# Performance work log

Measured on AMD Instinct MI355X. Metric: run time of the kernel, lower is better.

Reference implementation:

```python
import jax, jax.numpy as jnp
import numpy as np

GROUP_SIZES = np.array([64, 48, 56, 40, 32, 24, 16, 8])
N_GROUPS = 8
MAX_GS = 64
D_MODEL = 2048
BATCH = 8192


def setup_inputs() -> dict:
    key = jax.random.key(0)
    k1, k2, k3, k4 = jax.random.split(key, 4)
    hidden = jax.random.normal(k1, (BATCH, N_GROUPS, D_MODEL), dtype=jnp.float32)
    chosen = jax.random.randint(k2, (BATCH,), 0, N_GROUPS)
    scale = 1.0 / np.sqrt(D_MODEL)  # nn.Linear default init range
    W = jax.random.uniform(k3, (N_GROUPS, MAX_GS, D_MODEL), minval=-scale, maxval=scale, dtype=jnp.float32)
    b = jax.random.uniform(k4, (N_GROUPS, MAX_GS), minval=-scale, maxval=scale, dtype=jnp.float32)
    gs = jnp.asarray(GROUP_SIZES, dtype=jnp.int32)
    # zero-pad decoder rows beyond each group's true output size
    row_mask = jnp.arange(MAX_GS)[None, :] < gs[:, None]  # [G, MAX_GS]
    W = W * row_mask[:, :, None]
    b = b * row_mask
    return {"hidden": hidden, "chosen_group_idx": chosen, "W": W, "b": b, "group_sizes": gs}


def reference(hidden, chosen_group_idx, W, b, group_sizes):
    # hidden: [B, G, D]; chosen_group_idx: [B]; W: [G, MAX_GS, D] (zero-padded); b: [G, MAX_GS]
    # Gather each sample's chosen group slice: [B, D]
    h = jnp.take_along_axis(hidden, chosen_group_idx[:, None, None], axis=1)[:, 0, :]
    Wg = W[chosen_group_idx]  # [B, MAX_GS, D]
    bg = b[chosen_group_idx]  # [B, MAX_GS]
    preds = jnp.einsum('bd,bgd->bg', h, Wg) + bg  # [B, MAX_GS]
    valid = jnp.arange(W.shape[1])[None, :] < group_sizes[chosen_group_idx][:, None]
    preds = jnp.where(valid, preds, 0.0)  # padded slots are zero, as in the torch module
    return preds, valid
```

## Files before the change

kernel.cpp:

```cpp
#include <hip/hip_runtime.h>
#include <hip/hip_bf16.h>

#define BATCH   8192
#define NGRP    8
#define MAXGS   64
#define DMODEL  2048
#define TM      16
#define TILES   (BATCH / TM)
#define NBLK    32
#define NKK     (DMODEL / 32)

typedef __attribute__((ext_vector_type(8))) short  short8;
typedef __attribute__((ext_vector_type(4))) float  f32x4;
typedef __attribute__((ext_vector_type(4))) short  short4v;

#define CNT_OFF   0
#define HIST_OFF  512
#define BASES_OFF 1536
#define LISTS_OFF 4096
#define W_OFF     (LISTS_OFF + NGRP * BATCH * 4)
#define CNT_STRIDE 16

static __device__ __forceinline__ short bf(float f) {
    __hip_bfloat16 h = __float2bfloat16(f);
    return (short)__bfloat16_as_ushort(h);
}

__global__ __launch_bounds__(256) void init_hist_kernel(
    const float* __restrict__ W,
    const int* __restrict__ chosen,
    unsigned short* __restrict__ Wb2,
    int* __restrict__ hist)
{
    int blk = blockIdx.x;
    int tid = threadIdx.x;
    if (blk < 1024) {
        int e = (blk * 256 + tid) * 4;
        int g = e >> 17;
        int rem = e & ((MAXGS * DMODEL) - 1);
        int c = rem >> 11;
        int k = rem & (DMODEL - 1);
        int kk = k >> 5, j = k & 31;
        float4 w = *reinterpret_cast<const float4*>(W + e);
        ushort4 o;
        o.x = (unsigned short)bf(w.x); o.y = (unsigned short)bf(w.y);
        o.z = (unsigned short)bf(w.z); o.w = (unsigned short)bf(w.w);
        size_t dst = (((size_t)g * NKK + kk) * MAXGS + c) * 32 + j;
        *reinterpret_cast<ushort4*>(Wb2 + dst) = o;
    } else {
        int hb = blk - 1024;
        __shared__ int h[NGRP];
        if (tid < NGRP) h[tid] = 0;
        __syncthreads();
        int g = chosen[hb * 256 + tid];
        atomicAdd(&h[g], 1);
        __syncthreads();
        if (tid < NGRP) hist[hb * NGRP + tid] = h[tid];
    }
}

__global__ __launch_bounds__(64) void scan_kernel(const int* __restrict__ hist,
                                                  int* __restrict__ bases,
                                                  int* __restrict__ cnt) {
    int tid = threadIdx.x;
    if (tid < NGRP) {
        int s = 0;
        for (int blk = 0; blk < NBLK; ++blk) {
            bases[blk * NGRP + tid] = s;
            s += hist[blk * NGRP + tid];
        }
        cnt[tid * CNT_STRIDE] = s;
    }
}

__global__ __launch_bounds__(256) void scatter_kernel(const int* __restrict__ chosen,
                                                      const int* __restrict__ bases,
                                                      int* __restrict__ lists) {
    __shared__ int wcnt[4][NGRP];
    __shared__ int wbase[4][NGRP];
    int tid  = threadIdx.x;
    int blk  = blockIdx.x;
    int w    = tid >> 6;
    int lane = tid & 63;
    int b = blk * 256 + tid;
    int g = chosen[b];

    int rank = 0;
    unsigned long long below = (1ull << lane) - 1ull;
    #pragma unroll
    for (int gg = 0; gg < NGRP; ++gg) {
        unsigned long long m = __ballot(g == gg);
        if (g == gg) rank = __popcll(m & below);
        if (lane == gg) wcnt[w][gg] = __popcll(m);
    }
    __syncthreads();
    if (tid < NGRP) {
        int base = bases[blk * NGRP + tid];
        #pragma unroll
        for (int ww = 0; ww < 4; ++ww) {
            wbase[ww][tid] = base;
            base += wcnt[ww][tid];
        }
    }
    __syncthreads();
    lists[g * BATCH + wbase[w][g] + rank] = b;
}

__global__ __launch_bounds__(256, 2) void gemm_kernel(
    const float* __restrict__ hidden,
    const float* __restrict__ bias,
    const int* __restrict__ gsizes,
    const int* __restrict__ cnt,
    const int* __restrict__ lists,
    const unsigned short* __restrict__ Wb2,
    float* __restrict__ out)
{
    int bid = blockIdx.x;
    int g = bid & (NGRP - 1);
    int t = bid >> 3;
    int c = cnt[g * CNT_STRIDE];
    int m0 = t * TM;
    if (m0 >= c) return;

    __shared__ unsigned short A[TM][DMODEL];

    int tid  = threadIdx.x;
    int w    = tid >> 6;
    int lane = tid & 63;
    int lrow = lane & 15;
    int kg   = lane >> 4;

    {
        const float* src[4];
        #pragma unroll
        for (int i = 0; i < 4; ++i) {
            int m  = m0 + 4 * w + i;
            int ms = m < c ? m : c - 1;
            src[i] = hidden + ((size_t)lists[g * BATCH + ms] * NGRP + g) * DMODEL
                   + lane * 4;
        }
        f32x4 ra[8], rb[8];
        #pragma unroll
        for (int h = 0; h < 8; ++h)
            ra[h] = *reinterpret_cast<const f32x4*>(src[0] + h * 256);
        #pragma unroll
        for (int h = 0; h < 8; ++h)
            rb[h] = *reinterpret_cast<const f32x4*>(src[1] + h * 256);

        #pragma unroll
        for (int i = 0; i < 4; ++i) {
            int r = 4 * w + i;
            int swz = ((r & 7) << 4) | ((r & 1) << 6);
            char* abase = (char*)&A[r][0];
            #pragma unroll
            for (int h = 0; h < 8; ++h) {
                f32x4 v = ra[h];
                short4v o;
                o[0] = bf(v[0]); o[1] = bf(v[1]); o[2] = bf(v[2]); o[3] = bf(v[3]);
                int byte = (h * 512 + lane * 8) ^ swz;
                *reinterpret_cast<short4v*>(abase + byte) = o;
            }
            if (i < 3) {
                #pragma unroll
                for (int h = 0; h < 8; ++h) ra[h] = rb[h];
                if (i < 2) {
                    #pragma unroll
                    for (int h = 0; h < 8; ++h)
                        rb[h] = *reinterpret_cast<const f32x4*>(src[i + 2] + h * 256);
                }
            }
        }
    }
    __syncthreads();

    {
        int swzr = ((lrow & 7) << 4) | ((lrow & 1) << 6);
        const char* arow = (const char*)&A[lrow][0];
        const unsigned short* bp =
            Wb2 + (size_t)g * NKK * MAXGS * 32 + (w * 16 + lrow) * 32 + kg * 8;

        f32x4 acc = f32x4{0, 0, 0, 0};
        #pragma unroll 8
        for (int kk = 0; kk < NKK; ++kk) {
            int byte = (kk * 64 + kg * 16) ^ swzr;
            short8 af  = *reinterpret_cast<const short8*>(arow + byte);
            short8 bfr = *reinterpret_cast<const short8*>(bp + (size_t)kk * MAXGS * 32);
            acc = __builtin_amdgcn_mfma_f32_16x16x32_bf16(af, bfr, acc, 0, 0, 0);
        }

        int gsz = gsizes[g];
        int n = w * 16 + lrow;
        float bv = bias[g * MAXGS + n];
        #pragma unroll
        for (int r = 0; r < 4; ++r) {
            int m = m0 + kg * 4 + r;
            if (m < c) {
                int s = lists[g * BATCH + m];
                out[(size_t)s * MAXGS + n] = acc[r] + bv;
                out[(size_t)(BATCH + s) * MAXGS + n] = (n < gsz) ? 1.0f : 0.0f;
            }
        }
    }
}

extern "C" void kernel_launch(void* const* d_in, const int* in_sizes, int n_in,
                              void* d_out, int out_size, void* d_ws, size_t ws_size,
                              hipStream_t stream) {
    const float* hidden = (const float*)d_in[0];
    const int*   chosen = (const int*)d_in[1];
    const float* W      = (const float*)d_in[2];
    const float* bias   = (const float*)d_in[3];
    const int*   gs     = (const int*)d_in[4];
    float* out = (float*)d_out;

    char* ws = (char*)d_ws;
    int* cnt   = (int*)(ws + CNT_OFF);
    int* hist  = (int*)(ws + HIST_OFF);
    int* bases = (int*)(ws + BASES_OFF);
    int* lists = (int*)(ws + LISTS_OFF);
    unsigned short* Wb2 = (unsigned short*)(ws + W_OFF);

    init_hist_kernel<<<dim3(1024 + NBLK), dim3(256), 0, stream>>>(W, chosen, Wb2, hist);
    scan_kernel<<<dim3(1), dim3(64), 0, stream>>>(hist, bases, cnt);
    scatter_kernel<<<dim3(NBLK), dim3(256), 0, stream>>>(chosen, bases, lists);
    gemm_kernel<<<dim3(NGRP * TILES), dim3(256), 0, stream>>>(
        hidden, bias, gs, cnt, lists, Wb2, out);
}
```

Measured before the change: 38.16 us.

## Fuse scan into scatter and overlap second-half A loads with first-half MFMA

Removes the separate single-block scan kernel: each scatter block now computes its own prefix base from the histogram in shared memory, and block 0 writes the group totals. This saves one kernel launch on the critical path. The GEMM kernel splits the K dimension in half. Global loads for the second half of the gathered hidden rows are issued before the MFMA loop over the first half, then converted and written to LDS with an extra barrier, so load latency overlaps compute at the cost of more registers.

```diff
diff --git a/kernel.cpp b/kernel.cpp
--- a/kernel.cpp
+++ b/kernel.cpp
@@ -16,7 +16,6 @@
 
 #define CNT_OFF   0
 #define HIST_OFF  512
-#define BASES_OFF 1536
 #define LISTS_OFF 4096
 #define W_OFF     (LISTS_OFF + NGRP * BATCH * 4)
 #define CNT_STRIDE 16
@@ -59,32 +58,34 @@
     }
 }
 
-__global__ __launch_bounds__(64) void scan_kernel(const int* __restrict__ hist,
-                                                  int* __restrict__ bases,
-                                                  int* __restrict__ cnt) {
-    int tid = threadIdx.x;
-    if (tid < NGRP) {
-        int s = 0;
-        for (int blk = 0; blk < NBLK; ++blk) {
-            bases[blk * NGRP + tid] = s;
-            s += hist[blk * NGRP + tid];
-        }
-        cnt[tid * CNT_STRIDE] = s;
-    }
-}
-
 __global__ __launch_bounds__(256) void scatter_kernel(const int* __restrict__ chosen,
-                                                      const int* __restrict__ bases,
-                                                      int* __restrict__ lists) {
+                                                      const int* __restrict__ hist,
+                                                      int* __restrict__ lists,
+                                                      int* __restrict__ cnt) {
+    __shared__ int hloc[NBLK * NGRP];
+    __shared__ int gbase[NGRP];
     __shared__ int wcnt[4][NGRP];
     __shared__ int wbase[4][NGRP];
     int tid  = threadIdx.x;
     int blk  = blockIdx.x;
     int w    = tid >> 6;
     int lane = tid & 63;
+
+    if (tid < NBLK * NGRP) hloc[tid] = hist[tid];
+    __syncthreads();
+    if (tid < NGRP) {
+        int s = 0;
+        for (int b2 = 0; b2 < blk; ++b2) s += hloc[b2 * NGRP + tid];
+        gbase[tid] = s;
+        if (blk == 0) {
+            int tot = 0;
+            for (int b2 = 0; b2 < NBLK; ++b2) tot += hloc[b2 * NGRP + tid];
+            cnt[tid * CNT_STRIDE] = tot;
+        }
+    }
+
     int b = blk * 256 + tid;
     int g = chosen[b];
-
     int rank = 0;
     unsigned long long below = (1ull << lane) - 1ull;
     #pragma unroll
@@ -95,7 +96,7 @@
     }
     __syncthreads();
     if (tid < NGRP) {
-        int base = bases[blk * NGRP + tid];
+        int base = gbase[tid];
         #pragma unroll
         for (int ww = 0; ww < 4; ++ww) {
             wbase[ww][tid] = base;
@@ -130,30 +131,30 @@
     int lrow = lane & 15;
     int kg   = lane >> 4;
 
+    const float* src[4];
+    #pragma unroll
+    for (int i = 0; i < 4; ++i) {
+        int m  = m0 + 4 * w + i;
+        int ms = m < c ? m : c - 1;
+        src[i] = hidden + ((size_t)lists[g * BATCH + ms] * NGRP + g) * DMODEL
+               + lane * 4;
+    }
+
     {
-        const float* src[4];
-        #pragma unroll
-        for (int i = 0; i < 4; ++i) {
-            int m  = m0 + 4 * w + i;
-            int ms = m < c ? m : c - 1;
-            src[i] = hidden + ((size_t)lists[g * BATCH + ms] * NGRP + g) * DMODEL
-                   + lane * 4;
-        }
-        f32x4 ra[8], rb[8];
-        #pragma unroll
-        for (int h = 0; h < 8; ++h)
+        f32x4 ra[4], rb[4];
+        #pragma unroll
+        for (int h = 0; h < 4; ++h)
             ra[h] = *reinterpret_cast<const f32x4*>(src[0] + h * 256);
         #pragma unroll
-        for (int h = 0; h < 8; ++h)
+        for (int h = 0; h < 4; ++h)
             rb[h] = *reinterpret_cast<const f32x4*>(src[1] + h * 256);
-
         #pragma unroll
         for (int i = 0; i < 4; ++i) {
             int r = 4 * w + i;
             int swz = ((r & 7) << 4) | ((r & 1) << 6);
             char* abase = (char*)&A[r][0];
             #pragma unroll
-            for (int h = 0; h < 8; ++h) {
+            for (int h = 0; h < 4; ++h) {
                 f32x4 v = ra[h];
                 short4v o;
                 o[0] = bf(v[0]); o[1] = bf(v[1]); o[2] = bf(v[2]); o[3] = bf(v[3]);
@@ -162,43 +163,80 @@
             }
             if (i < 3) {
                 #pragma unroll
-                for (int h = 0; h < 8; ++h) ra[h] = rb[h];
+                for (int h = 0; h < 4; ++h) ra[h] = rb[h];
                 if (i < 2) {
                     #pragma unroll
-                    for (int h = 0; h < 8; ++h)
+                    for (int h = 0; h < 4; ++h)
                         rb[h] = *reinterpret_cast<const f32x4*>(src[i + 2] + h * 256);
                 }
             }
         }
     }
-    __syncthreads();
-
-    {
-        int swzr = ((lrow & 7) << 4) | ((lrow & 1) << 6);
-        const char* arow = (const char*)&A[lrow][0];
-        const unsigned short* bp =
-            Wb2 + (size_t)g * NKK * MAXGS * 32 + (w * 16 + lrow) * 32 + kg * 8;
-
-        f32x4 acc = f32x4{0, 0, 0, 0};
-        #pragma unroll 8
-        for (int kk = 0; kk < NKK; ++kk) {
-            int byte = (kk * 64 + kg * 16) ^ swzr;
-            short8 af  = *reinterpret_cast<const short8*>(arow + byte);
-            short8 bfr = *reinterpret_cast<const short8*>(bp + (size_t)kk * MAXGS * 32);
-            acc = __builtin_amdgcn_mfma_f32_16x16x32_bf16(af, bfr, acc, 0, 0, 0);
-        }
-
-        int gsz = gsizes[g];
-        int n = w * 16 + lrow;
-        float bv = bias[g * MAXGS + n];
-        #pragma unroll
-        for (int r = 0; r < 4; ++r) {
-            int m = m0 + kg * 4 + r;
-            if (m < c) {
-                int s = lists[g * BATCH + m];
-                out[(size_t)s * MAXGS + n] = acc[r] + bv;
-                out[(size_t)(BATCH + s) * MAXGS + n] = (n < gsz) ? 1.0f : 0.0f;
-            }
+
+    f32x4 rc[16];
+    #pragma unroll
+    for (int i = 0; i < 4; ++i)
+        #pragma unroll
+        for (int h = 0; h < 4; ++h)
+            rc[i * 4 + h] = *reinterpret_cast<const f32x4*>(src[i] + 1024 + h * 256);
+    __builtin_amdgcn_sched_barrier(0);
+
+    asm volatile("s_waitcnt lgkmcnt(0)" ::: "memory");
+    __builtin_amdgcn_s_barrier();
+    __builtin_amdgcn_sched_barrier(0);
+
+    int swzr = ((lrow & 7) << 4) | ((lrow & 1) << 6);
+    const char* arow = (const char*)&A[lrow][0];
+    const unsigned short* bp =
+        Wb2 + (size_t)g * NKK * MAXGS * 32 + (w * 16 + lrow) * 32 + kg * 8;
+
+    f32x4 acc = f32x4{0, 0, 0, 0};
+
+    #pragma unroll 8
+    for (int kk = 0; kk < NKK / 2; ++kk) {
+        int byte = (kk * 64 + kg * 16) ^ swzr;
+        short8 af  = *reinterpret_cast<const short8*>(arow + byte);
+        short8 bfr = *reinterpret_cast<const short8*>(bp + (size_t)kk * MAXGS * 32);
+        acc = __builtin_amdgcn_mfma_f32_16x16x32_bf16(af, bfr, acc, 0, 0, 0);
+    }
+
+    asm volatile("s_waitcnt vmcnt(0)" ::: "memory");
+    #pragma unroll
+    for (int i = 0; i < 4; ++i) {
+        int r = 4 * w + i;
+        int swz = ((r & 7) << 4) | ((r & 1) << 6);
+        char* abase = (char*)&A[r][0];
+        #pragma unroll
+        for (int h = 0; h < 4; ++h) {
+            f32x4 v = rc[i * 4 + h];
+            short4v o;
+            o[0] = bf(v[0]); o[1] = bf(v[1]); o[2] = bf(v[2]); o[3] = bf(v[3]);
+            int byte = (2048 + h * 512 + lane * 8) ^ swz;
+            *reinterpret_cast<short4v*>(abase + byte) = o;
+        }
+    }
+    asm volatile("s_waitcnt lgkmcnt(0)" ::: "memory");
+    __builtin_amdgcn_s_barrier();
+    __builtin_amdgcn_sched_barrier(0);
+
+    #pragma unroll 8
+    for (int kk = NKK / 2; kk < NKK; ++kk) {
+        int byte = (kk * 64 + kg * 16) ^ swzr;
+        short8 af  = *reinterpret_cast<const short8*>(arow + byte);
+        short8 bfr = *reinterpret_cast<const short8*>(bp + (size_t)kk * MAXGS * 32);
+        acc = __builtin_amdgcn_mfma_f32_16x16x32_bf16(af, bfr, acc, 0, 0, 0);
+    }
+
+    int gsz = gsizes[g];
+    int n = w * 16 + lrow;
+    float bv = bias[g * MAXGS + n];
+    #pragma unroll
+    for (int r = 0; r < 4; ++r) {
+        int m = m0 + kg * 4 + r;
+        if (m < c) {
+            int s = lists[g * BATCH + m];
+            out[(size_t)s * MAXGS + n] = acc[r] + bv;
+            out[(size_t)(BATCH + s) * MAXGS + n] = (n < gsz) ? 1.0f : 0.0f;
         }
     }
 }
@@ -216,13 +254,11 @@
     char* ws = (char*)d_ws;
     int* cnt   = (int*)(ws + CNT_OFF);
     int* hist  = (int*)(ws + HIST_OFF);
-    int* bases = (int*)(ws + BASES_OFF);
     int* lists = (int*)(ws + LISTS_OFF);
     unsigned short* Wb2 = (unsigned short*)(ws + W_OFF);
 
     init_hist_kernel<<<dim3(1024 + NBLK), dim3(256), 0, stream>>>(W, chosen, Wb2, hist);
-    scan_kernel<<<dim3(1), dim3(64), 0, stream>>>(hist, bases, cnt);
-    scatter_kernel<<<dim3(NBLK), dim3(256), 0, stream>>>(chosen, bases, lists);
+    scatter_kernel<<<dim3(NBLK), dim3(256), 0, stream>>>(chosen, hist, lists, cnt);
     gemm_kernel<<<dim3(NGRP * TILES), dim3(256), 0, stream>>>(
         hidden, bias, gs, cnt, lists, Wb2, out);
 }
```

Result: faster. 36.18 us (-5.2%).

## Fold scan into scatter and warp-specialize GEMM with double-buffered K chunks

Applied to the files above, without the earlier changes.

Removes the separate single-block scan kernel: each scatter block loads the histogram into shared memory and computes its own prefix base, and block 0 writes the group totals. The GEMM kernel grows to 512 threads, split into 4 producer waves that load hidden rows and convert them to bf16 into a double-buffered 512-wide K chunk, and 4 consumer waves that run the MFMA loop over each chunk. The goal is one fewer kernel launch and overlap of the gather/convert with MFMA compute, in exchange for barriers at every chunk and a larger block with fewer registers per thread.

```diff
diff --git a/kernel.cpp b/kernel.cpp
--- a/kernel.cpp
+++ b/kernel.cpp
@@ -9,14 +9,15 @@
 #define TILES   (BATCH / TM)
 #define NBLK    32
 #define NKK     (DMODEL / 32)
+#define KC      512
+#define NPH     (DMODEL / KC)
+#define KKP     (KC / 32)
 
 typedef __attribute__((ext_vector_type(8))) short  short8;
 typedef __attribute__((ext_vector_type(4))) float  f32x4;
-typedef __attribute__((ext_vector_type(4))) short  short4v;
 
 #define CNT_OFF   0
 #define HIST_OFF  512
-#define BASES_OFF 1536
 #define LISTS_OFF 4096
 #define W_OFF     (LISTS_OFF + NGRP * BATCH * 4)
 #define CNT_STRIDE 16
@@ -59,32 +60,34 @@
     }
 }
 
-__global__ __launch_bounds__(64) void scan_kernel(const int* __restrict__ hist,
-                                                  int* __restrict__ bases,
-                                                  int* __restrict__ cnt) {
-    int tid = threadIdx.x;
-    if (tid < NGRP) {
-        int s = 0;
-        for (int blk = 0; blk < NBLK; ++blk) {
-            bases[blk * NGRP + tid] = s;
-            s += hist[blk * NGRP + tid];
-        }
-        cnt[tid * CNT_STRIDE] = s;
-    }
-}
-
 __global__ __launch_bounds__(256) void scatter_kernel(const int* __restrict__ chosen,
-                                                      const int* __restrict__ bases,
-                                                      int* __restrict__ lists) {
+                                                      const int* __restrict__ hist,
+                                                      int* __restrict__ lists,
+                                                      int* __restrict__ cnt) {
+    __shared__ int hloc[NBLK * NGRP];
+    __shared__ int gbase[NGRP];
     __shared__ int wcnt[4][NGRP];
     __shared__ int wbase[4][NGRP];
     int tid  = threadIdx.x;
     int blk  = blockIdx.x;
     int w    = tid >> 6;
     int lane = tid & 63;
+
+    if (tid < NBLK * NGRP) hloc[tid] = hist[tid];
+    __syncthreads();
+    if (tid < NGRP) {
+        int s = 0;
+        for (int b2 = 0; b2 < blk; ++b2) s += hloc[b2 * NGRP + tid];
+        gbase[tid] = s;
+        if (blk == 0) {
+            int tot = 0;
+            for (int b2 = 0; b2 < NBLK; ++b2) tot += hloc[b2 * NGRP + tid];
+            cnt[tid * CNT_STRIDE] = tot;
+        }
+    }
+
     int b = blk * 256 + tid;
     int g = chosen[b];
-
     int rank = 0;
     unsigned long long below = (1ull << lane) - 1ull;
     #pragma unroll
@@ -95,7 +98,7 @@
     }
     __syncthreads();
     if (tid < NGRP) {
-        int base = bases[blk * NGRP + tid];
+        int base = gbase[tid];
         #pragma unroll
         for (int ww = 0; ww < 4; ++ww) {
             wbase[ww][tid] = base;
@@ -106,7 +109,12 @@
     lists[g * BATCH + wbase[w][g] + rank] = b;
 }
 
-__global__ __launch_bounds__(256, 2) void gemm_kernel(
+#define LGKM0_BAR()                                          \
+    asm volatile("s_waitcnt lgkmcnt(0)" ::: "memory");       \
+    __builtin_amdgcn_s_barrier();                            \
+    __builtin_amdgcn_sched_barrier(0)
+
+__global__ __launch_bounds__(512, 2) void gemm_kernel(
     const float* __restrict__ hidden,
     const float* __restrict__ bias,
     const int* __restrict__ gsizes,
@@ -122,74 +130,76 @@
     int m0 = t * TM;
     if (m0 >= c) return;
 
-    __shared__ unsigned short A[TM][DMODEL];
+    __shared__ unsigned short A[2][TM][KC];
 
     int tid  = threadIdx.x;
     int w    = tid >> 6;
     int lane = tid & 63;
-    int lrow = lane & 15;
-    int kg   = lane >> 4;
-
-    {
+
+    if (w < 4) {
         const float* src[4];
         #pragma unroll
         for (int i = 0; i < 4; ++i) {
             int m  = m0 + 4 * w + i;
             int ms = m < c ? m : c - 1;
             src[i] = hidden + ((size_t)lists[g * BATCH + ms] * NGRP + g) * DMODEL
-                   + lane * 4;
-        }
-        f32x4 ra[8], rb[8];
-        #pragma unroll
-        for (int h = 0; h < 8; ++h)
-            ra[h] = *reinterpret_cast<const f32x4*>(src[0] + h * 256);
-        #pragma unroll
-        for (int h = 0; h < 8; ++h)
-            rb[h] = *reinterpret_cast<const f32x4*>(src[1] + h * 256);
-
-        #pragma unroll
-        for (int i = 0; i < 4; ++i) {
-            int r = 4 * w + i;
-            int swz = ((r & 7) << 4) | ((r & 1) << 6);
-            char* abase = (char*)&A[r][0];
+                   + lane * 8;
+        }
+        #define PRODUCE(buf, ph)                                               \
+            {                                                                  \
+                f32x4 v0[4], v1[4];                                            \
+                _Pragma("unroll")                                              \
+                for (int i = 0; i < 4; ++i) {                                  \
+                    v0[i] = *reinterpret_cast<const f32x4*>(src[i] + (ph) * KC);     \
+                    v1[i] = *reinterpret_cast<const f32x4*>(src[i] + (ph) * KC + 4); \
+                }                                                              \
+                _Pragma("unroll")                                              \
+                for (int i = 0; i < 4; ++i) {                                  \
+                    int r = 4 * w + i;                                         \
+                    int swz = ((r & 7) << 4) | ((r & 1) << 6);                 \
+                    short8 o;                                                  \
+                    o[0] = bf(v0[i][0]); o[1] = bf(v0[i][1]);                  \
+                    o[2] = bf(v0[i][2]); o[3] = bf(v0[i][3]);                  \
+                    o[4] = bf(v1[i][0]); o[5] = bf(v1[i][1]);                  \
+                    o[6] = bf(v1[i][2]); o[7] = bf(v1[i][3]);                  \
+                    char* ab = (char*)&A[buf][r][0];                           \
+                    *reinterpret_cast<short8*>(ab + ((lane * 16) ^ swz)) = o;  \
+                }                                                              \
+            }
+        PRODUCE(0, 0)
+        LGKM0_BAR();
+        #pragma unroll
+        for (int ch = 0; ch < NPH; ++ch) {
+            if (ch + 1 < NPH) PRODUCE((ch + 1) & 1, ch + 1)
+            LGKM0_BAR();
+        }
+        #undef PRODUCE
+    } else {
+        int cw   = w - 4;
+        int lrow = lane & 15;
+        int kg   = lane >> 4;
+        int swzr = ((lrow & 7) << 4) | ((lrow & 1) << 6);
+        const unsigned short* bp =
+            Wb2 + (size_t)g * NKK * MAXGS * 32 + (cw * 16 + lrow) * 32 + kg * 8;
+
+        f32x4 acc = f32x4{0, 0, 0, 0};
+        LGKM0_BAR();
+        #pragma unroll
+        for (int ch = 0; ch < NPH; ++ch) {
+            const char* arow = (const char*)&A[ch & 1][lrow][0];
             #pragma unroll
-            for (int h = 0; h < 8; ++h) {
-                f32x4 v = ra[h];
-                short4v o;
-                o[0] = bf(v[0]); o[1] = bf(v[1]); o[2] = bf(v[2]); o[3] = bf(v[3]);
-                int byte = (h * 512 + lane * 8) ^ swz;
-                *reinterpret_cast<short4v*>(abase + byte) = o;
+            for (int k2 = 0; k2 < KKP; ++k2) {
+                int byte = (k2 * 64 + kg * 16) ^ swzr;
+                short8 af  = *reinterpret_cast<const short8*>(arow + byte);
+                short8 bfr = *reinterpret_cast<const short8*>(
+                    bp + (size_t)(ch * KKP + k2) * MAXGS * 32);
+                acc = __builtin_amdgcn_mfma_f32_16x16x32_bf16(af, bfr, acc, 0, 0, 0);
             }
-            if (i < 3) {
-                #pragma unroll
-                for (int h = 0; h < 8; ++h) ra[h] = rb[h];
-                if (i < 2) {
-                    #pragma unroll
-                    for (int h = 0; h < 8; ++h)
-                        rb[h] = *reinterpret_cast<const f32x4*>(src[i + 2] + h * 256);
-                }
-            }
-        }
-    }
-    __syncthreads();
-
-    {
-        int swzr = ((lrow & 7) << 4) | ((lrow & 1) << 6);
-        const char* arow = (const char*)&A[lrow][0];
-        const unsigned short* bp =
-            Wb2 + (size_t)g * NKK * MAXGS * 32 + (w * 16 + lrow) * 32 + kg * 8;
-
-        f32x4 acc = f32x4{0, 0, 0, 0};
-        #pragma unroll 8
-        for (int kk = 0; kk < NKK; ++kk) {
-            int byte = (kk * 64 + kg * 16) ^ swzr;
-            short8 af  = *reinterpret_cast<const short8*>(arow + byte);
-            short8 bfr = *reinterpret_cast<const short8*>(bp + (size_t)kk * MAXGS * 32);
-            acc = __builtin_amdgcn_mfma_f32_16x16x32_bf16(af, bfr, acc, 0, 0, 0);
+            LGKM0_BAR();
         }
 
         int gsz = gsizes[g];
-        int n = w * 16 + lrow;
+        int n = cw * 16 + lrow;
         float bv = bias[g * MAXGS + n];
         #pragma unroll
         for (int r = 0; r < 4; ++r) {
@@ -216,13 +226,11 @@
     char* ws = (char*)d_ws;
     int* cnt   = (int*)(ws + CNT_OFF);
     int* hist  = (int*)(ws + HIST_OFF);
-    int* bases = (int*)(ws + BASES_OFF);
     int* lists = (int*)(ws + LISTS_OFF);
     unsigned short* Wb2 = (unsigned short*)(ws + W_OFF);
 
     init_hist_kernel<<<dim3(1024 + NBLK), dim3(256), 0, stream>>>(W, chosen, Wb2, hist);
-    scan_kernel<<<dim3(1), dim3(64), 0, stream>>>(hist, bases, cnt);
-    scatter_kernel<<<dim3(NBLK), dim3(256), 0, stream>>>(chosen, bases, lists);
-    gemm_kernel<<<dim3(NGRP * TILES), dim3(256), 0, stream>>>(
+    scatter_kernel<<<dim3(NBLK), dim3(256), 0, stream>>>(chosen, hist, lists, cnt);
+    gemm_kernel<<<dim3(NGRP * TILES), dim3(512), 0, stream>>>(
         hidden, bias, gs, cnt, lists, Wb2, out);
 }
```

New measurement: 35.86 us. 1.06x faster.

## Fold scan into scatter and launch GEMM over a compacted tile map

Applied to the files above, without the earlier changes.

The single-thread scan kernel is removed. Each scatter block now recomputes its per-group prefix bases from the histogram in shared memory, and block 0 also writes the group counts. Block 0 additionally builds a compact list of (group, tile) work items, so the GEMM launches at most 520 blocks instead of 4096, most of which used to exit immediately. This drops one kernel launch and avoids scheduling thousands of empty blocks, at the cost of redundant prefix sums in every scatter block and a serial map-build step in block 0.

```diff
diff --git a/kernel.cpp b/kernel.cpp
--- a/kernel.cpp
+++ b/kernel.cpp
@@ -6,9 +6,9 @@
 #define MAXGS   64
 #define DMODEL  2048
 #define TM      16
-#define TILES   (BATCH / TM)
 #define NBLK    32
 #define NKK     (DMODEL / 32)
+#define MAXTILES 520
 
 typedef __attribute__((ext_vector_type(8))) short  short8;
 typedef __attribute__((ext_vector_type(4))) float  f32x4;
@@ -16,7 +16,7 @@
 
 #define CNT_OFF   0
 #define HIST_OFF  512
-#define BASES_OFF 1536
+#define MAP_OFF   1536
 #define LISTS_OFF 4096
 #define W_OFF     (LISTS_OFF + NGRP * BATCH * 4)
 #define CNT_STRIDE 16
@@ -59,32 +59,54 @@
     }
 }
 
-__global__ __launch_bounds__(64) void scan_kernel(const int* __restrict__ hist,
-                                                  int* __restrict__ bases,
-                                                  int* __restrict__ cnt) {
-    int tid = threadIdx.x;
-    if (tid < NGRP) {
-        int s = 0;
-        for (int blk = 0; blk < NBLK; ++blk) {
-            bases[blk * NGRP + tid] = s;
-            s += hist[blk * NGRP + tid];
-        }
-        cnt[tid * CNT_STRIDE] = s;
-    }
-}
-
 __global__ __launch_bounds__(256) void scatter_kernel(const int* __restrict__ chosen,
-                                                      const int* __restrict__ bases,
-                                                      int* __restrict__ lists) {
+                                                      const int* __restrict__ hist,
+                                                      int* __restrict__ lists,
+                                                      int* __restrict__ cnt,
+                                                      int* __restrict__ map) {
+    __shared__ int hloc[NBLK * NGRP];
+    __shared__ int gbase[NGRP];
+    __shared__ int ntl[NGRP];
     __shared__ int wcnt[4][NGRP];
     __shared__ int wbase[4][NGRP];
     int tid  = threadIdx.x;
     int blk  = blockIdx.x;
     int w    = tid >> 6;
     int lane = tid & 63;
+
+    if (tid < NBLK * NGRP) hloc[tid] = hist[tid];
+    __syncthreads();
+    if (tid < NGRP) {
+        int s = 0;
+        for (int b2 = 0; b2 < blk; ++b2) s += hloc[b2 * NGRP + tid];
+        gbase[tid] = s;
+        int tot = s;
+        for (int b2 = blk; b2 < NBLK; ++b2) tot += hloc[b2 * NGRP + tid];
+        ntl[tid] = (tot + TM - 1) / TM;
+        if (blk == 0) cnt[tid * CNT_STRIDE] = tot;
+    }
+    __syncthreads();
+
+    if (blk == 0) {
+        for (int q = tid; q < MAXTILES; q += 256) map[q] = -1;
+        __syncthreads();
+        for (int p = tid; p < NGRP * 512; p += 256) {
+            int t = p >> 3, gg = p & 7;
+            if (t < ntl[gg]) {
+                int pos = 0;
+                #pragma unroll
+                for (int g2 = 0; g2 < NGRP; ++g2) {
+                    int nt = ntl[g2];
+                    pos += (t < nt ? t : nt);
+                    pos += (g2 < gg && nt > t) ? 1 : 0;
+                }
+                map[pos] = (gg << 16) | t;
+            }
+        }
+    }
+
     int b = blk * 256 + tid;
     int g = chosen[b];
-
     int rank = 0;
     unsigned long long below = (1ull << lane) - 1ull;
     #pragma unroll
@@ -95,7 +117,7 @@
     }
     __syncthreads();
     if (tid < NGRP) {
-        int base = bases[blk * NGRP + tid];
+        int base = gbase[tid];
         #pragma unroll
         for (int ww = 0; ww < 4; ++ww) {
             wbase[ww][tid] = base;
@@ -112,15 +134,16 @@
     const int* __restrict__ gsizes,
     const int* __restrict__ cnt,
     const int* __restrict__ lists,
+    const int* __restrict__ map,
     const unsigned short* __restrict__ Wb2,
     float* __restrict__ out)
 {
-    int bid = blockIdx.x;
-    int g = bid & (NGRP - 1);
-    int t = bid >> 3;
+    int e = map[blockIdx.x];
+    if (e < 0) return;
+    int g = e >> 16;
+    int t = e & 0xFFFF;
     int c = cnt[g * CNT_STRIDE];
     int m0 = t * TM;
-    if (m0 >= c) return;
 
     __shared__ unsigned short A[TM][DMODEL];
 
@@ -216,13 +239,12 @@
     char* ws = (char*)d_ws;
     int* cnt   = (int*)(ws + CNT_OFF);
     int* hist  = (int*)(ws + HIST_OFF);
-    int* bases = (int*)(ws + BASES_OFF);
+    int* map   = (int*)(ws + MAP_OFF);
     int* lists = (int*)(ws + LISTS_OFF);
     unsigned short* Wb2 = (unsigned short*)(ws + W_OFF);
 
     init_hist_kernel<<<dim3(1024 + NBLK), dim3(256), 0, stream>>>(W, chosen, Wb2, hist);
-    scan_kernel<<<dim3(1), dim3(64), 0, stream>>>(hist, bases, cnt);
-    scatter_kernel<<<dim3(NBLK), dim3(256), 0, stream>>>(chosen, bases, lists);
-    gemm_kernel<<<dim3(NGRP * TILES), dim3(256), 0, stream>>>(
-        hidden, bias, gs, cnt, lists, Wb2, out);
-}
+    scatter_kernel<<<dim3(NBLK), dim3(256), 0, stream>>>(chosen, hist, lists, cnt, map);
+    gemm_kernel<<<dim3(MAXTILES), dim3(256), 0, stream>>>(
+        hidden, bias, gs, cnt, lists, map, Wb2, out);
+}
```

Measured after the change: 38.29 us. Within noise of the previous version (+0.3%).
